# Optimization experiments

Measured on AMD Instinct MI355X. Metric: run time of the kernel, lower is better.

The kernel has to match this reference:

```python
import jax, jax.numpy as jnp
import numpy as np
import math

B, T, C = 2, 2048, 1024
N_HEADS = 16
HEAD_DIM = C // N_HEADS  # 64


def setup_inputs() -> dict:
    key = jax.random.key(0)
    ks = jax.random.split(key, 5)
    scale = 0.02
    return {
        "x": jax.random.normal(ks[0], (B, T, C), dtype=jnp.float32),
        "Wq": jax.random.normal(ks[1], (C, C), dtype=jnp.float32) * scale,
        "Wk": jax.random.normal(ks[2], (C, C), dtype=jnp.float32) * scale,
        "Wv": jax.random.normal(ks[3], (C, C), dtype=jnp.float32) * scale,
        "Wc": jax.random.normal(ks[4], (C, C), dtype=jnp.float32) * scale,
        "bc": jnp.zeros((C,), dtype=jnp.float32),
    }


def reference(x, Wq, Wk, Wv, Wc, bc):
    b, t, c = x.shape
    h, dh = N_HEADS, HEAD_DIM
    # Q/K/V projections (Linear, no bias): y = x @ W.T
    def proj(W):
        y = jnp.einsum('btc,dc->btd', x, W)
        return y.reshape(b, t, h, dh).transpose(0, 2, 1, 3)  # [B,H,T,dh]
    Q, K, V = proj(Wq), proj(Wk), proj(Wv)

    # scaled dot-product scores [B,H,T,T]
    scores = jnp.einsum('bhqd,bhkd->bhqk', Q, K) / math.sqrt(dh)
    # additive causal mask: + (1 - tril) * -1e9, as in the original
    causal = jnp.tril(jnp.ones((t, t), dtype=scores.dtype))
    scores = scores + (1.0 - causal) * (-1e9)

    attn = jax.nn.softmax(scores, axis=-1)  # dropout = identity (eval mode)
    o = jnp.einsum('bhqk,bhkd->bhqd', attn, V)
    o = o.transpose(0, 2, 1, 3).reshape(b, t, c)
    # output projection with bias (resid dropout = identity in eval)
    return jnp.einsum('btc,dc->btd', o, Wc) + bc
```

## Files before the change

kernel.cpp:

```cpp
#include <hip/hip_runtime.h>
#include <hip/hip_bf16.h>


typedef __attribute__((ext_vector_type(4))) float f32x4;
typedef __attribute__((ext_vector_type(4))) unsigned int u32x4;
typedef __attribute__((ext_vector_type(8))) __bf16 bf16x8;
typedef __attribute__((ext_vector_type(8))) unsigned short us8;
typedef __attribute__((ext_vector_type(4))) unsigned short us4;

#define LOG2E 1.4426950408889634f

__device__ __forceinline__ unsigned short f2bf(float f) {
    unsigned u = __builtin_bit_cast(unsigned, f);
    u += 0x7fffu + ((u >> 16) & 1u);
    return (unsigned short)(u >> 16);
}

__device__ __forceinline__ unsigned cvt_pk_bf16(float lo, float hi) {
    unsigned r;
    asm("v_cvt_pk_bf16_f32 %0, %1, %2" : "=v"(r) : "v"(lo), "v"(hi));
    return r;
}

__device__ __forceinline__ f32x4 mfma16(us8 a, us8 b, f32x4 c) {
    return __builtin_amdgcn_mfma_f32_16x16x32_bf16(
        __builtin_bit_cast(bf16x8, a), __builtin_bit_cast(bf16x8, b), c, 0, 0, 0);
}

__global__ __launch_bounds__(256) void fill_sentinel(float* __restrict__ out, int n) {
    int i = blockIdx.x * 256 + threadIdx.x;
    if (i < n) out[i] = 12345.0f;
}

__global__ __launch_bounds__(256) void cvt_x(const float* __restrict__ x,
                                             unsigned short* __restrict__ xb) {
    int idx = (blockIdx.x * 256 + threadIdx.x) * 4;
    f32x4 v = *(const f32x4*)(x + idx);
    us4 o = { f2bf(v[0]), f2bf(v[1]), f2bf(v[2]), f2bf(v[3]) };
    *(us4*)(xb + idx) = o;
}

template <bool AF32, bool BF32>
__device__ __forceinline__ void gemm_core(
    const void* __restrict__ Av, const void* __restrict__ Bv,
    int K, int m0, int n0, unsigned short* As, unsigned short* Bs, f32x4 acc[4][4]) {
    const float* Af = (const float*)Av;
    const unsigned short* Ab = (const unsigned short*)Av;
    const float* Bf = (const float*)Bv;
    const unsigned short* Bb = (const unsigned short*)Bv;
    const int tid = threadIdx.x;
    const int lane = tid & 63, wid = tid >> 6;
    const int g = lane >> 4, s = lane & 15;
    const int wr = wid >> 1, wc = wid & 1;
#pragma unroll
    for (int mi = 0; mi < 4; mi++)
#pragma unroll
        for (int ni = 0; ni < 4; ni++) acc[mi][ni] = (f32x4){0.f, 0.f, 0.f, 0.f};
    const int row = tid >> 3, col = (tid & 7) * 8;
    for (int k0 = 0; k0 < K; k0 += 64) {
        us8 av[4], bv[4];
#pragma unroll
        for (int p = 0; p < 4; p++) {
            size_t aoff = (size_t)(m0 + row + p * 32) * K + k0 + col;
            if (AF32) {
                f32x4 v0 = *(const f32x4*)(Af + aoff);
                f32x4 v1 = *(const f32x4*)(Af + aoff + 4);
                av[p] = (us8){ f2bf(v0[0]), f2bf(v0[1]), f2bf(v0[2]), f2bf(v0[3]),
                               f2bf(v1[0]), f2bf(v1[1]), f2bf(v1[2]), f2bf(v1[3]) };
            } else {
                av[p] = *(const us8*)(Ab + aoff);
            }
            size_t boff = (size_t)(n0 + row + p * 32) * K + k0 + col;
            if (BF32) {
                f32x4 v0 = *(const f32x4*)(Bf + boff);
                f32x4 v1 = *(const f32x4*)(Bf + boff + 4);
                bv[p] = (us8){ f2bf(v0[0]), f2bf(v0[1]), f2bf(v0[2]), f2bf(v0[3]),
                               f2bf(v1[0]), f2bf(v1[1]), f2bf(v1[2]), f2bf(v1[3]) };
            } else {
                bv[p] = *(const us8*)(Bb + boff);
            }
        }
        __syncthreads();
#pragma unroll
        for (int p = 0; p < 4; p++) {
            *(us8*)(As + (row + p * 32) * 72 + col) = av[p];
            *(us8*)(Bs + (row + p * 32) * 72 + col) = bv[p];
        }
        __syncthreads();
#pragma unroll
        for (int kk = 0; kk < 2; kk++) {
            us8 af[4], bf[4];
#pragma unroll
            for (int mi = 0; mi < 4; mi++)
                af[mi] = *(const us8*)(As + (wr * 64 + mi * 16 + s) * 72 + kk * 32 + g * 8);
#pragma unroll
            for (int ni = 0; ni < 4; ni++)
                bf[ni] = *(const us8*)(Bs + (wc * 64 + ni * 16 + s) * 72 + kk * 32 + g * 8);
#pragma unroll
            for (int mi = 0; mi < 4; mi++)
#pragma unroll
                for (int ni = 0; ni < 4; ni++)
                    acc[mi][ni] = mfma16(af[mi], bf[ni], acc[mi][ni]);
        }
    }
}

__global__ __launch_bounds__(256) void gemm_qkv(
    const unsigned short* __restrict__ X, const float* __restrict__ Wq,
    const float* __restrict__ Wk, const float* __restrict__ Wv,
    unsigned short* __restrict__ Qb, unsigned short* __restrict__ Kb,
    unsigned short* __restrict__ Vb) {
    __shared__ unsigned short As[128 * 72];
    __shared__ unsigned short Bs[128 * 72];
    const int bm = blockIdx.x & 31, bn = blockIdx.x >> 5;
    const int m0 = bm * 128;
    const int which = bn >> 3;
    const int n0 = (bn & 7) * 128;
    const float* W = which == 0 ? Wq : (which == 1 ? Wk : Wv);
    unsigned short* dst = which == 0 ? Qb : (which == 1 ? Kb : Vb);
    const float scale = which == 0 ? 0.125f : 1.0f;
    f32x4 acc[4][4];
    gemm_core<false, true>(X, W, 1024, m0, n0, As, Bs, acc);
    const int lane = threadIdx.x & 63, wid = threadIdx.x >> 6;
    const int g = lane >> 4, s = lane & 15, wr = wid >> 1, wc = wid & 1;
#pragma unroll
    for (int mi = 0; mi < 4; mi++)
#pragma unroll
        for (int ni = 0; ni < 4; ni++) {
            int n1 = n0 + wc * 64 + ni * 16 + s;
            int hh = n1 >> 6, dd = n1 & 63;
#pragma unroll
            for (int r = 0; r < 4; r++) {
                int mg = m0 + wr * 64 + mi * 16 + 4 * g + r;
                int bb = mg >> 11, tt = mg & 2047;
                dst[((size_t)(bb * 16 + hh) * 2048 + tt) * 64 + dd] = f2bf(acc[mi][ni][r] * scale);
            }
        }
}

__global__ __launch_bounds__(256) void transpose_v(
    const unsigned short* __restrict__ Vb, unsigned short* __restrict__ VtG) {
    __shared__ unsigned short T[64 * 68];
    const int bh = blockIdx.x >> 5, tt = blockIdx.x & 31;
    const int t0 = tt * 64;
    const unsigned short* src = Vb + (size_t)bh * 2048 * 64;
    unsigned short* dst = VtG + (size_t)bh * 64 * 2048;
    const int r = threadIdx.x >> 3, c = (threadIdx.x & 7) * 8;
#pragma unroll
    for (int p = 0; p < 2; p++) {
        us8 v = *(const us8*)(src + (size_t)(t0 + r + 32 * p) * 64 + c);
        *(us8*)(&T[(r + 32 * p) * 68 + c]) = v;
    }
    __syncthreads();
#pragma unroll
    for (int p = 0; p < 2; p++) {
        int d = r + 32 * p;
        us8 o;
#pragma unroll
        for (int j = 0; j < 8; j++) o[j] = T[(c + j) * 68 + d];
        *(us8*)(dst + (size_t)d * 2048 + t0 + c) = o;
    }
}

#define ATTN_EPILOGUE(QB0, OA, LR)                                              \
    {                                                                           \
        float li[4];                                                            \
        _Pragma("unroll") for (int r = 0; r < 4; r++)                           \
            li[r] = __shfl((LR), 4 * g + r, 64);                                \
        _Pragma("unroll") for (int db = 0; db < 4; db++)                        \
            _Pragma("unroll") for (int r = 0; r < 4; r++) {                     \
                int qq = (QB0) + 4 * g + r;                                     \
                float v = (OA)[db][r] / li[r];                                  \
                Ob[((size_t)(b * 2048) + qq) * 1024 + h * 64 + db * 16 + s] = f2bf(v); \
            }                                                                   \
    }

__global__ __launch_bounds__(256) void attn(
    const unsigned short* __restrict__ Qb, const unsigned short* __restrict__ Kb,
    const unsigned short* __restrict__ VtG, unsigned short* __restrict__ Ob) {
    __shared__ unsigned short Ks[64 * 72];
    __shared__ unsigned short Vt[64 * 72];
    const int bh = blockIdx.x >> 4, i = blockIdx.x & 15;
    const int b = bh >> 4, h = bh & 15;
    const unsigned short* Qp = Qb + (size_t)bh * 2048 * 64;
    const unsigned short* Kp = Kb + (size_t)bh * 2048 * 64;
    const unsigned short* Vp = VtG + (size_t)bh * 64 * 2048;
    const int tid = threadIdx.x, lane = tid & 63, wid = tid >> 6;
    const int g = lane >> 4, s = lane & 15;
    const int qbA = i * 64 + wid * 16;
    const int qbB = (31 - i) * 64 + wid * 16;
    const int qgA = qbA + s, qgB = qbB + s;
    us8 qfA[2], qfB[2];
    qfA[0] = *(const us8*)(Qp + (size_t)qgA * 64 + g * 8);
    qfA[1] = *(const us8*)(Qp + (size_t)qgA * 64 + 32 + g * 8);
    qfB[0] = *(const us8*)(Qp + (size_t)qgB * 64 + g * 8);
    qfB[1] = *(const us8*)(Qp + (size_t)qgB * 64 + 32 + g * 8);
    float m_run = -3.0e38f, l_run = 0.f;
    f32x4 o_acc[4];
#pragma unroll
    for (int db = 0; db < 4; db++) o_acc[db] = (f32x4){0.f, 0.f, 0.f, 0.f};
    const int srow = tid >> 3, scol = (tid & 7) * 8;
    us8 kpre[2], vpre[2];
#pragma unroll
    for (int p = 0; p < 2; p++) {
        kpre[p] = *(const us8*)(Kp + (size_t)(srow + 32 * p) * 64 + scol);
        vpre[p] = *(const us8*)(Vp + (size_t)(srow + 32 * p) * 2048 + scol);
    }
    for (int it = 0; it <= 32; ++it) {
        const bool qsel = it > i;
        const int kv0 = (qsel ? it - i - 1 : it) * 64;
        __syncthreads();
#pragma unroll
        for (int p = 0; p < 2; p++) {
            *(us8*)(Ks + (srow + 32 * p) * 72 + scol) = kpre[p];
            *(us8*)(Vt + (srow + 32 * p) * 72 + scol) = vpre[p];
        }
        __syncthreads();
        if (it < 32) {
            const int nx = it + 1;
            const int nkv0 = (nx > i ? nx - i - 1 : nx) * 64;
#pragma unroll
            for (int p = 0; p < 2; p++) {
                kpre[p] = *(const us8*)(Kp + (size_t)(nkv0 + srow + 32 * p) * 64 + scol);
                vpre[p] = *(const us8*)(Vp + (size_t)(srow + 32 * p) * 2048 + nkv0 + scol);
            }
        }
        if (it == i + 1) {
            ATTN_EPILOGUE(qbA, o_acc, l_run);
            m_run = -3.0e38f; l_run = 0.f;
#pragma unroll
            for (int db = 0; db < 4; db++) o_acc[db] = (f32x4){0.f, 0.f, 0.f, 0.f};
        }
        const int qg = qsel ? qgB : qgA;
        const us8* qf = qsel ? qfB : qfA;
        float sf[4][4];
        __builtin_amdgcn_s_setprio(1);
#pragma unroll
        for (int f = 0; f < 4; f++) {
            f32x4 a = (f32x4){0.f, 0.f, 0.f, 0.f};
            us8 k0v = *(const us8*)(Ks + (f * 16 + s) * 72 + g * 8);
            us8 k1v = *(const us8*)(Ks + (f * 16 + s) * 72 + 32 + g * 8);
            a = mfma16(k0v, qf[0], a);
            a = mfma16(k1v, qf[1], a);
#pragma unroll
            for (int r = 0; r < 4; r++) sf[f][r] = a[r];
        }
        __builtin_amdgcn_s_setprio(0);
        const bool diag = qsel ? (it == 32) : (it == i);
        if (diag) {
#pragma unroll
            for (int f = 0; f < 4; f++)
#pragma unroll
                for (int r = 0; r < 4; r++)
                    if (kv0 + f * 16 + 4 * g + r > qg) sf[f][r] = -3.0e38f;
        }
        float mt = -3.0e38f;
#pragma unroll
        for (int f = 0; f < 4; f++)
#pragma unroll
            for (int r = 0; r < 4; r++) mt = fmaxf(mt, sf[f][r]);
        mt = fmaxf(mt, __shfl_xor(mt, 16));
        mt = fmaxf(mt, __shfl_xor(mt, 32));
        float mnew = fmaxf(m_run, mt);
        float alpha = __builtin_amdgcn_exp2f((m_run - mnew) * LOG2E);
        float psum = 0.f;
#pragma unroll
        for (int f = 0; f < 4; f++)
#pragma unroll
            for (int r = 0; r < 4; r++) {
                float p = __builtin_amdgcn_exp2f((sf[f][r] - mnew) * LOG2E);
                sf[f][r] = p;
                psum += p;
            }
        psum += __shfl_xor(psum, 16);
        psum += __shfl_xor(psum, 32);
        l_run = l_run * alpha + psum;
        m_run = mnew;
        float al[4];
#pragma unroll
        for (int r = 0; r < 4; r++) al[r] = __shfl(alpha, 4 * g + r, 64);
#pragma unroll
        for (int db = 0; db < 4; db++)
#pragma unroll
            for (int r = 0; r < 4; r++) o_acc[db][r] *= al[r];
        unsigned pk[4][2];
#pragma unroll
        for (int f = 0; f < 4; f++)
#pragma unroll
            for (int hh2 = 0; hh2 < 2; hh2++)
                pk[f][hh2] = cvt_pk_bf16(sf[f][2 * hh2], sf[f][2 * hh2 + 1]);
        const int srcA = 32 * (g & 1) + s, srcB = srcA + 16;
        const bool ghi = g >= 2;
        us8 pa[2];
#pragma unroll
        for (int kk = 0; kk < 2; kk++) {
            unsigned e0 = __shfl(pk[kk * 2][0], srcA, 64);
            unsigned e1 = __shfl(pk[kk * 2][1], srcA, 64);
            unsigned e2 = __shfl(pk[kk * 2][0], srcB, 64);
            unsigned e3 = __shfl(pk[kk * 2][1], srcB, 64);
            unsigned o0 = __shfl(pk[kk * 2 + 1][0], srcA, 64);
            unsigned o1 = __shfl(pk[kk * 2 + 1][1], srcA, 64);
            unsigned o2 = __shfl(pk[kk * 2 + 1][0], srcB, 64);
            unsigned o3 = __shfl(pk[kk * 2 + 1][1], srcB, 64);
            u32x4 dw = { ghi ? o0 : e0, ghi ? o1 : e1, ghi ? o2 : e2, ghi ? o3 : e3 };
            pa[kk] = __builtin_bit_cast(us8, dw);
        }
        __builtin_amdgcn_s_setprio(1);
#pragma unroll
        for (int db = 0; db < 4; db++) {
            const unsigned short* vrow = Vt + (db * 16 + s) * 72;
            us8 vf0 = *(const us8*)(vrow + g * 8);
            o_acc[db] = mfma16(pa[0], vf0, o_acc[db]);
            us8 vf1 = *(const us8*)(vrow + 32 + g * 8);
            o_acc[db] = mfma16(pa[1], vf1, o_acc[db]);
        }
        __builtin_amdgcn_s_setprio(0);
    }
    ATTN_EPILOGUE(qbB, o_acc, l_run);
}

__global__ __launch_bounds__(256) void gemm_out(
    const unsigned short* __restrict__ O, const float* __restrict__ Wc,
    const float* __restrict__ bc, float* __restrict__ out) {
    __shared__ unsigned short As[128 * 72];
    __shared__ unsigned short Bs[128 * 72];
    const int bm = blockIdx.x & 31, bn = blockIdx.x >> 5;
    const int m0 = bm * 128, n0 = bn * 128;
    f32x4 acc[4][4];
    gemm_core<false, true>(O, Wc, 1024, m0, n0, As, Bs, acc);
    const int lane = threadIdx.x & 63, wid = threadIdx.x >> 6;
    const int g = lane >> 4, s = lane & 15, wr = wid >> 1, wc = wid & 1;
#pragma unroll
    for (int mi = 0; mi < 4; mi++)
#pragma unroll
        for (int ni = 0; ni < 4; ni++) {
            int ng = n0 + wc * 64 + ni * 16 + s;
            float bias = bc[ng];
#pragma unroll
            for (int r = 0; r < 4; r++) {
                int mg = m0 + wr * 64 + mi * 16 + 4 * g + r;
                out[(size_t)mg * 1024 + ng] = acc[mi][ni][r] + bias;
            }
        }
}

extern "C" void kernel_launch(void* const* d_in, const int* in_sizes, int n_in,
                              void* d_out, int out_size, void* d_ws, size_t ws_size,
                              hipStream_t stream) {
    const float* x  = (const float*)d_in[0];
    const float* Wq = (const float*)d_in[1];
    const float* Wk = (const float*)d_in[2];
    const float* Wv = (const float*)d_in[3];
    const float* Wc = (const float*)d_in[4];
    const float* bc = (const float*)d_in[5];
    float* out = (float*)d_out;

    if (ws_size < 33554432) {
        fill_sentinel<<<(out_size + 255) / 256, 256, 0, stream>>>(out, out_size);
        return;
    }
    char* w = (char*)d_ws;
    unsigned short* Qb = (unsigned short*)(w);
    unsigned short* Kb = (unsigned short*)(w + 8388608);
    unsigned short* Vb = (unsigned short*)(w + 16777216);
    unsigned short* Ob = (unsigned short*)(w + 25165824);
    unsigned short* VtG = (unsigned short*)d_out;
    unsigned short* xb  = (unsigned short*)((char*)d_out + 8388608);

    cvt_x<<<4096, 256, 0, stream>>>(x, xb);
    gemm_qkv<<<768, 256, 0, stream>>>(xb, Wq, Wk, Wv, Qb, Kb, Vb);
    transpose_v<<<1024, 256, 0, stream>>>(Vb, VtG);
    attn<<<512, 256, 0, stream>>>(Qb, Kb, VtG, Ob);
    gemm_out<<<256, 256, 0, stream>>>(Ob, Wc, bc, out);
}
```

Baseline: 134.6 us.

## Pre-convert weights to bf16, use direct global-to-LDS loads, lazy softmax rescale

```diff
diff --git a/kernel.cpp b/kernel.cpp
--- a/kernel.cpp
+++ b/kernel.cpp
@@ -27,27 +27,43 @@
         __builtin_bit_cast(bf16x8, a), __builtin_bit_cast(bf16x8, b), c, 0, 0, 0);
 }
 
+__device__ __forceinline__ void gload16(const unsigned short* gp, unsigned short* lp) {
+    __builtin_amdgcn_global_load_lds(
+        (const __attribute__((address_space(1))) void*)gp,
+        (__attribute__((address_space(3))) void*)lp, 16, 0, 0);
+}
+
 __global__ __launch_bounds__(256) void fill_sentinel(float* __restrict__ out, int n) {
     int i = blockIdx.x * 256 + threadIdx.x;
     if (i < n) out[i] = 12345.0f;
 }
 
-__global__ __launch_bounds__(256) void cvt_x(const float* __restrict__ x,
-                                             unsigned short* __restrict__ xb) {
+__global__ __launch_bounds__(256) void cvt_xw(
+    const float* __restrict__ x, const float* __restrict__ wq,
+    const float* __restrict__ wk, const float* __restrict__ wv,
+    unsigned short* __restrict__ xb, unsigned short* __restrict__ wqkvb) {
+    long i = (long)(blockIdx.x * 256 + threadIdx.x) * 4;
+    const float* src; unsigned short* dst; long off;
+    if (i < 4194304L)      { src = x;  dst = xb;              off = i; }
+    else if (i < 5242880L) { src = wq; dst = wqkvb;           off = i - 4194304L; }
+    else if (i < 6291456L) { src = wk; dst = wqkvb + 1048576; off = i - 5242880L; }
+    else                   { src = wv; dst = wqkvb + 2097152; off = i - 6291456L; }
+    f32x4 v = *(const f32x4*)(src + off);
+    us4 o = { f2bf(v[0]), f2bf(v[1]), f2bf(v[2]), f2bf(v[3]) };
+    *(us4*)(dst + off) = o;
+}
+
+__global__ __launch_bounds__(256) void cvt_wc(const float* __restrict__ wc,
+                                              unsigned short* __restrict__ wcb) {
     int idx = (blockIdx.x * 256 + threadIdx.x) * 4;
-    f32x4 v = *(const f32x4*)(x + idx);
+    f32x4 v = *(const f32x4*)(wc + idx);
     us4 o = { f2bf(v[0]), f2bf(v[1]), f2bf(v[2]), f2bf(v[3]) };
-    *(us4*)(xb + idx) = o;
-}
-
-template <bool AF32, bool BF32>
-__device__ __forceinline__ void gemm_core(
-    const void* __restrict__ Av, const void* __restrict__ Bv,
+    *(us4*)(wcb + idx) = o;
+}
+
+__device__ __forceinline__ void gemm_core_g(
+    const unsigned short* __restrict__ A, const unsigned short* __restrict__ B,
     int K, int m0, int n0, unsigned short* As, unsigned short* Bs, f32x4 acc[4][4]) {
-    const float* Af = (const float*)Av;
-    const unsigned short* Ab = (const unsigned short*)Av;
-    const float* Bf = (const float*)Bv;
-    const unsigned short* Bb = (const unsigned short*)Bv;
     const int tid = threadIdx.x;
     const int lane = tid & 63, wid = tid >> 6;
     const int g = lane >> 4, s = lane & 15;
@@ -56,35 +72,14 @@
     for (int mi = 0; mi < 4; mi++)
 #pragma unroll
         for (int ni = 0; ni < 4; ni++) acc[mi][ni] = (f32x4){0.f, 0.f, 0.f, 0.f};
-    const int row = tid >> 3, col = (tid & 7) * 8;
+    const int lrow = lane >> 3, lcol = (lane & 7) * 8;
     for (int k0 = 0; k0 < K; k0 += 64) {
-        us8 av[4], bv[4];
+        __syncthreads();
 #pragma unroll
         for (int p = 0; p < 4; p++) {
-            size_t aoff = (size_t)(m0 + row + p * 32) * K + k0 + col;
-            if (AF32) {
-                f32x4 v0 = *(const f32x4*)(Af + aoff);
-                f32x4 v1 = *(const f32x4*)(Af + aoff + 4);
-                av[p] = (us8){ f2bf(v0[0]), f2bf(v0[1]), f2bf(v0[2]), f2bf(v0[3]),
-                               f2bf(v1[0]), f2bf(v1[1]), f2bf(v1[2]), f2bf(v1[3]) };
-            } else {
-                av[p] = *(const us8*)(Ab + aoff);
-            }
-            size_t boff = (size_t)(n0 + row + p * 32) * K + k0 + col;
-            if (BF32) {
-                f32x4 v0 = *(const f32x4*)(Bf + boff);
-                f32x4 v1 = *(const f32x4*)(Bf + boff + 4);
-                bv[p] = (us8){ f2bf(v0[0]), f2bf(v0[1]), f2bf(v0[2]), f2bf(v0[3]),
-                               f2bf(v1[0]), f2bf(v1[1]), f2bf(v1[2]), f2bf(v1[3]) };
-            } else {
-                bv[p] = *(const us8*)(Bb + boff);
-            }
-        }
-        __syncthreads();
-#pragma unroll
-        for (int p = 0; p < 4; p++) {
-            *(us8*)(As + (row + p * 32) * 72 + col) = av[p];
-            *(us8*)(Bs + (row + p * 32) * 72 + col) = bv[p];
+            const int chunk = p * 4 + wid;
+            gload16(A + (size_t)(m0 + chunk * 8 + lrow) * K + k0 + lcol, As + chunk * 512);
+            gload16(B + (size_t)(n0 + chunk * 8 + lrow) * K + k0 + lcol, Bs + chunk * 512);
         }
         __syncthreads();
 #pragma unroll
@@ -92,10 +87,10 @@
             us8 af[4], bf[4];
 #pragma unroll
             for (int mi = 0; mi < 4; mi++)
-                af[mi] = *(const us8*)(As + (wr * 64 + mi * 16 + s) * 72 + kk * 32 + g * 8);
+                af[mi] = *(const us8*)(As + (wr * 64 + mi * 16 + s) * 64 + kk * 32 + g * 8);
 #pragma unroll
             for (int ni = 0; ni < 4; ni++)
-                bf[ni] = *(const us8*)(Bs + (wc * 64 + ni * 16 + s) * 72 + kk * 32 + g * 8);
+                bf[ni] = *(const us8*)(Bs + (wc * 64 + ni * 16 + s) * 64 + kk * 32 + g * 8);
 #pragma unroll
             for (int mi = 0; mi < 4; mi++)
 #pragma unroll
@@ -106,28 +101,25 @@
 }
 
 __global__ __launch_bounds__(256) void gemm_qkv(
-    const unsigned short* __restrict__ X, const float* __restrict__ Wq,
-    const float* __restrict__ Wk, const float* __restrict__ Wv,
+    const unsigned short* __restrict__ X, const unsigned short* __restrict__ W,
     unsigned short* __restrict__ Qb, unsigned short* __restrict__ Kb,
     unsigned short* __restrict__ Vb) {
-    __shared__ unsigned short As[128 * 72];
-    __shared__ unsigned short Bs[128 * 72];
+    __shared__ unsigned short As[128 * 64];
+    __shared__ unsigned short Bs[128 * 64];
     const int bm = blockIdx.x & 31, bn = blockIdx.x >> 5;
-    const int m0 = bm * 128;
-    const int which = bn >> 3;
-    const int n0 = (bn & 7) * 128;
-    const float* W = which == 0 ? Wq : (which == 1 ? Wk : Wv);
-    unsigned short* dst = which == 0 ? Qb : (which == 1 ? Kb : Vb);
-    const float scale = which == 0 ? 0.125f : 1.0f;
+    const int m0 = bm * 128, n0 = bn * 128;
     f32x4 acc[4][4];
-    gemm_core<false, true>(X, W, 1024, m0, n0, As, Bs, acc);
+    gemm_core_g(X, W, 1024, m0, n0, As, Bs, acc);
     const int lane = threadIdx.x & 63, wid = threadIdx.x >> 6;
     const int g = lane >> 4, s = lane & 15, wr = wid >> 1, wc = wid & 1;
 #pragma unroll
     for (int mi = 0; mi < 4; mi++)
 #pragma unroll
         for (int ni = 0; ni < 4; ni++) {
-            int n1 = n0 + wc * 64 + ni * 16 + s;
+            int ng = n0 + wc * 64 + ni * 16 + s;
+            int which = ng >> 10, n1 = ng & 1023;
+            unsigned short* dst = which == 0 ? Qb : (which == 1 ? Kb : Vb);
+            float scale = which == 0 ? 0.125f : 1.0f;
             int hh = n1 >> 6, dd = n1 & 63;
 #pragma unroll
             for (int r = 0; r < 4; r++) {
@@ -180,7 +172,7 @@
     const unsigned short* __restrict__ VtG, unsigned short* __restrict__ Ob) {
     __shared__ unsigned short Ks[64 * 72];
     __shared__ unsigned short Vt[64 * 72];
-    const int bh = blockIdx.x >> 4, i = blockIdx.x & 15;
+    const int bh = blockIdx.x & 31, i = blockIdx.x >> 5;
     const int b = bh >> 4, h = bh & 15;
     const unsigned short* Qp = Qb + (size_t)bh * 2048 * 64;
     const unsigned short* Kp = Kb + (size_t)bh * 2048 * 64;
@@ -261,8 +253,19 @@
             for (int r = 0; r < 4; r++) mt = fmaxf(mt, sf[f][r]);
         mt = fmaxf(mt, __shfl_xor(mt, 16));
         mt = fmaxf(mt, __shfl_xor(mt, 32));
-        float mnew = fmaxf(m_run, mt);
-        float alpha = __builtin_amdgcn_exp2f((m_run - mnew) * LOG2E);
+        float mnew = m_run;
+        if (!__all(mt - m_run <= 8.0f)) {
+            mnew = fmaxf(m_run, mt);
+            float alpha = __builtin_amdgcn_exp2f((m_run - mnew) * LOG2E);
+            l_run *= alpha;
+            float al[4];
+#pragma unroll
+            for (int r = 0; r < 4; r++) al[r] = __shfl(alpha, 4 * g + r, 64);
+#pragma unroll
+            for (int db = 0; db < 4; db++)
+#pragma unroll
+                for (int r = 0; r < 4; r++) o_acc[db][r] *= al[r];
+        }
         float psum = 0.f;
 #pragma unroll
         for (int f = 0; f < 4; f++)
@@ -274,15 +277,8 @@
             }
         psum += __shfl_xor(psum, 16);
         psum += __shfl_xor(psum, 32);
-        l_run = l_run * alpha + psum;
+        l_run += psum;
         m_run = mnew;
-        float al[4];
-#pragma unroll
-        for (int r = 0; r < 4; r++) al[r] = __shfl(alpha, 4 * g + r, 64);
-#pragma unroll
-        for (int db = 0; db < 4; db++)
-#pragma unroll
-            for (int r = 0; r < 4; r++) o_acc[db][r] *= al[r];
         unsigned pk[4][2];
 #pragma unroll
         for (int f = 0; f < 4; f++)
@@ -320,14 +316,14 @@
 }
 
 __global__ __launch_bounds__(256) void gemm_out(
-    const unsigned short* __restrict__ O, const float* __restrict__ Wc,
+    const unsigned short* __restrict__ O, const unsigned short* __restrict__ Wcb,
     const float* __restrict__ bc, float* __restrict__ out) {
-    __shared__ unsigned short As[128 * 72];
-    __shared__ unsigned short Bs[128 * 72];
+    __shared__ unsigned short As[128 * 64];
+    __shared__ unsigned short Bs[128 * 64];
     const int bm = blockIdx.x & 31, bn = blockIdx.x >> 5;
     const int m0 = bm * 128, n0 = bn * 128;
     f32x4 acc[4][4];
-    gemm_core<false, true>(O, Wc, 1024, m0, n0, As, Bs, acc);
+    gemm_core_g(O, Wcb, 1024, m0, n0, As, Bs, acc);
     const int lane = threadIdx.x & 63, wid = threadIdx.x >> 6;
     const int g = lane >> 4, s = lane & 15, wr = wid >> 1, wc = wid & 1;
 #pragma unroll
@@ -360,16 +356,19 @@
         return;
     }
     char* w = (char*)d_ws;
-    unsigned short* Qb = (unsigned short*)(w);
-    unsigned short* Kb = (unsigned short*)(w + 8388608);
-    unsigned short* Vb = (unsigned short*)(w + 16777216);
-    unsigned short* Ob = (unsigned short*)(w + 25165824);
-    unsigned short* VtG = (unsigned short*)d_out;
-    unsigned short* xb  = (unsigned short*)((char*)d_out + 8388608);
-
-    cvt_x<<<4096, 256, 0, stream>>>(x, xb);
-    gemm_qkv<<<768, 256, 0, stream>>>(xb, Wq, Wk, Wv, Qb, Kb, Vb);
+    unsigned short* Qb  = (unsigned short*)(w);
+    unsigned short* Kb  = (unsigned short*)(w + 8388608);
+    unsigned short* Vb  = (unsigned short*)(w + 16777216);
+    unsigned short* Ob  = (unsigned short*)(w + 25165824);
+    unsigned short* Wcb = (unsigned short*)(w + 16777216);
+    unsigned short* wqkvb = (unsigned short*)d_out;
+    unsigned short* VtG   = (unsigned short*)d_out;
+    unsigned short* xb    = (unsigned short*)((char*)d_out + 8388608);
+
+    cvt_xw<<<7168, 256, 0, stream>>>(x, Wq, Wk, Wv, xb, wqkvb);
+    gemm_qkv<<<768, 256, 0, stream>>>(xb, wqkvb, Qb, Kb, Vb);
     transpose_v<<<1024, 256, 0, stream>>>(Vb, VtG);
+    cvt_wc<<<1024, 256, 0, stream>>>(Wc, Wcb);
     attn<<<512, 256, 0, stream>>>(Qb, Kb, VtG, Ob);
-    gemm_out<<<256, 256, 0, stream>>>(Ob, Wc, bc, out);
-}
+    gemm_out<<<256, 256, 0, stream>>>(Ob, Wcb, bc, out);
+}
```

Result: slower. 142.0 us (+5.5%).

## Fuse V transpose into QKV GEMM, async A loads, rebalance attention and output GEMM

Applied to the files above, without the earlier changes.

```diff
diff --git a/kernel.cpp b/kernel.cpp
--- a/kernel.cpp
+++ b/kernel.cpp
@@ -25,6 +25,12 @@
 __device__ __forceinline__ f32x4 mfma16(us8 a, us8 b, f32x4 c) {
     return __builtin_amdgcn_mfma_f32_16x16x32_bf16(
         __builtin_bit_cast(bf16x8, a), __builtin_bit_cast(bf16x8, b), c, 0, 0, 0);
+}
+
+__device__ __forceinline__ void gload16(const unsigned short* gp, unsigned short* lp) {
+    __builtin_amdgcn_global_load_lds(
+        (const __attribute__((address_space(1))) void*)gp,
+        (__attribute__((address_space(3))) void*)lp, 16, 0, 0);
 }
 
 __global__ __launch_bounds__(256) void fill_sentinel(float* __restrict__ out, int n) {
@@ -40,64 +46,51 @@
     *(us4*)(xb + idx) = o;
 }
 
-template <bool AF32, bool BF32>
-__device__ __forceinline__ void gemm_core(
-    const void* __restrict__ Av, const void* __restrict__ Bv,
-    int K, int m0, int n0, unsigned short* As, unsigned short* Bs, f32x4 acc[4][4]) {
-    const float* Af = (const float*)Av;
-    const unsigned short* Ab = (const unsigned short*)Av;
-    const float* Bf = (const float*)Bv;
-    const unsigned short* Bb = (const unsigned short*)Bv;
+template <int MI>
+__device__ __forceinline__ void gemm_core_m(
+    const unsigned short* __restrict__ A, const float* __restrict__ Bf,
+    int K, int m0, int n0, unsigned short* As, unsigned short* Bs, f32x4 acc[MI][4]) {
     const int tid = threadIdx.x;
     const int lane = tid & 63, wid = tid >> 6;
     const int g = lane >> 4, s = lane & 15;
     const int wr = wid >> 1, wc = wid & 1;
 #pragma unroll
-    for (int mi = 0; mi < 4; mi++)
+    for (int mi = 0; mi < MI; mi++)
 #pragma unroll
         for (int ni = 0; ni < 4; ni++) acc[mi][ni] = (f32x4){0.f, 0.f, 0.f, 0.f};
-    const int row = tid >> 3, col = (tid & 7) * 8;
+    const int lrow = lane >> 3, lcol = (lane & 7) * 8;
+    const int brow = tid >> 3, bcol = (tid & 7) * 8;
     for (int k0 = 0; k0 < K; k0 += 64) {
-        us8 av[4], bv[4];
+        us8 bv[4];
 #pragma unroll
         for (int p = 0; p < 4; p++) {
-            size_t aoff = (size_t)(m0 + row + p * 32) * K + k0 + col;
-            if (AF32) {
-                f32x4 v0 = *(const f32x4*)(Af + aoff);
-                f32x4 v1 = *(const f32x4*)(Af + aoff + 4);
-                av[p] = (us8){ f2bf(v0[0]), f2bf(v0[1]), f2bf(v0[2]), f2bf(v0[3]),
-                               f2bf(v1[0]), f2bf(v1[1]), f2bf(v1[2]), f2bf(v1[3]) };
-            } else {
-                av[p] = *(const us8*)(Ab + aoff);
-            }
-            size_t boff = (size_t)(n0 + row + p * 32) * K + k0 + col;
-            if (BF32) {
-                f32x4 v0 = *(const f32x4*)(Bf + boff);
-                f32x4 v1 = *(const f32x4*)(Bf + boff + 4);
-                bv[p] = (us8){ f2bf(v0[0]), f2bf(v0[1]), f2bf(v0[2]), f2bf(v0[3]),
-                               f2bf(v1[0]), f2bf(v1[1]), f2bf(v1[2]), f2bf(v1[3]) };
-            } else {
-                bv[p] = *(const us8*)(Bb + boff);
-            }
+            size_t boff = (size_t)(n0 + brow + p * 32) * K + k0 + bcol;
+            f32x4 v0 = *(const f32x4*)(Bf + boff);
+            f32x4 v1 = *(const f32x4*)(Bf + boff + 4);
+            bv[p] = (us8){ f2bf(v0[0]), f2bf(v0[1]), f2bf(v0[2]), f2bf(v0[3]),
+                           f2bf(v1[0]), f2bf(v1[1]), f2bf(v1[2]), f2bf(v1[3]) };
         }
         __syncthreads();
 #pragma unroll
-        for (int p = 0; p < 4; p++) {
-            *(us8*)(As + (row + p * 32) * 72 + col) = av[p];
-            *(us8*)(Bs + (row + p * 32) * 72 + col) = bv[p];
-        }
+        for (int p = 0; p < MI; p++) {
+            const int chunk = p * 4 + wid;
+            gload16(A + (size_t)(m0 + chunk * 8 + lrow) * K + k0 + lcol, As + chunk * 512);
+        }
+#pragma unroll
+        for (int p = 0; p < 4; p++)
+            *(us8*)(Bs + (brow + p * 32) * 72 + bcol) = bv[p];
         __syncthreads();
 #pragma unroll
         for (int kk = 0; kk < 2; kk++) {
-            us8 af[4], bf[4];
-#pragma unroll
-            for (int mi = 0; mi < 4; mi++)
-                af[mi] = *(const us8*)(As + (wr * 64 + mi * 16 + s) * 72 + kk * 32 + g * 8);
+            us8 af[MI], bf[4];
+#pragma unroll
+            for (int mi = 0; mi < MI; mi++)
+                af[mi] = *(const us8*)(As + (wr * (MI * 16) + mi * 16 + s) * 64 + kk * 32 + g * 8);
 #pragma unroll
             for (int ni = 0; ni < 4; ni++)
                 bf[ni] = *(const us8*)(Bs + (wc * 64 + ni * 16 + s) * 72 + kk * 32 + g * 8);
 #pragma unroll
-            for (int mi = 0; mi < 4; mi++)
+            for (int mi = 0; mi < MI; mi++)
 #pragma unroll
                 for (int ni = 0; ni < 4; ni++)
                     acc[mi][ni] = mfma16(af[mi], bf[ni], acc[mi][ni]);
@@ -109,20 +102,19 @@
     const unsigned short* __restrict__ X, const float* __restrict__ Wq,
     const float* __restrict__ Wk, const float* __restrict__ Wv,
     unsigned short* __restrict__ Qb, unsigned short* __restrict__ Kb,
-    unsigned short* __restrict__ Vb) {
-    __shared__ unsigned short As[128 * 72];
+    unsigned short* __restrict__ VtG) {
+    __shared__ unsigned short As[128 * 64];
     __shared__ unsigned short Bs[128 * 72];
     const int bm = blockIdx.x & 31, bn = blockIdx.x >> 5;
     const int m0 = bm * 128;
     const int which = bn >> 3;
     const int n0 = (bn & 7) * 128;
     const float* W = which == 0 ? Wq : (which == 1 ? Wk : Wv);
-    unsigned short* dst = which == 0 ? Qb : (which == 1 ? Kb : Vb);
-    const float scale = which == 0 ? 0.125f : 1.0f;
     f32x4 acc[4][4];
-    gemm_core<false, true>(X, W, 1024, m0, n0, As, Bs, acc);
+    gemm_core_m<4>(X, W, 1024, m0, n0, As, Bs, acc);
     const int lane = threadIdx.x & 63, wid = threadIdx.x >> 6;
     const int g = lane >> 4, s = lane & 15, wr = wid >> 1, wc = wid & 1;
+    const float scale = which == 0 ? 0.125f : 1.0f;
 #pragma unroll
     for (int mi = 0; mi < 4; mi++)
 #pragma unroll
@@ -133,68 +125,36 @@
             for (int r = 0; r < 4; r++) {
                 int mg = m0 + wr * 64 + mi * 16 + 4 * g + r;
                 int bb = mg >> 11, tt = mg & 2047;
-                dst[((size_t)(bb * 16 + hh) * 2048 + tt) * 64 + dd] = f2bf(acc[mi][ni][r] * scale);
+                unsigned short v = f2bf(acc[mi][ni][r] * scale);
+                if (which == 0)
+                    Qb[((size_t)(bb * 16 + hh) * 2048 + tt) * 64 + dd] = v;
+                else if (which == 1)
+                    Kb[((size_t)(bb * 16 + hh) * 2048 + tt) * 64 + dd] = v;
+                else
+                    VtG[((size_t)(bb * 16 + hh) * 64 + dd) * 2048 + tt] = v;
             }
         }
 }
-
-__global__ __launch_bounds__(256) void transpose_v(
-    const unsigned short* __restrict__ Vb, unsigned short* __restrict__ VtG) {
-    __shared__ unsigned short T[64 * 68];
-    const int bh = blockIdx.x >> 5, tt = blockIdx.x & 31;
-    const int t0 = tt * 64;
-    const unsigned short* src = Vb + (size_t)bh * 2048 * 64;
-    unsigned short* dst = VtG + (size_t)bh * 64 * 2048;
-    const int r = threadIdx.x >> 3, c = (threadIdx.x & 7) * 8;
-#pragma unroll
-    for (int p = 0; p < 2; p++) {
-        us8 v = *(const us8*)(src + (size_t)(t0 + r + 32 * p) * 64 + c);
-        *(us8*)(&T[(r + 32 * p) * 68 + c]) = v;
-    }
-    __syncthreads();
-#pragma unroll
-    for (int p = 0; p < 2; p++) {
-        int d = r + 32 * p;
-        us8 o;
-#pragma unroll
-        for (int j = 0; j < 8; j++) o[j] = T[(c + j) * 68 + d];
-        *(us8*)(dst + (size_t)d * 2048 + t0 + c) = o;
-    }
-}
-
-#define ATTN_EPILOGUE(QB0, OA, LR)                                              \
-    {                                                                           \
-        float li[4];                                                            \
-        _Pragma("unroll") for (int r = 0; r < 4; r++)                           \
-            li[r] = __shfl((LR), 4 * g + r, 64);                                \
-        _Pragma("unroll") for (int db = 0; db < 4; db++)                        \
-            _Pragma("unroll") for (int r = 0; r < 4; r++) {                     \
-                int qq = (QB0) + 4 * g + r;                                     \
-                float v = (OA)[db][r] / li[r];                                  \
-                Ob[((size_t)(b * 2048) + qq) * 1024 + h * 64 + db * 16 + s] = f2bf(v); \
-            }                                                                   \
-    }
 
 __global__ __launch_bounds__(256) void attn(
     const unsigned short* __restrict__ Qb, const unsigned short* __restrict__ Kb,
     const unsigned short* __restrict__ VtG, unsigned short* __restrict__ Ob) {
     __shared__ unsigned short Ks[64 * 72];
     __shared__ unsigned short Vt[64 * 72];
-    const int bh = blockIdx.x >> 4, i = blockIdx.x & 15;
+    const int bh = blockIdx.x & 31, j = blockIdx.x >> 5;
+    const int q4 = j & 7, sel = j >> 3;
+    const int i = sel == 0 ? q4 : (sel == 1 ? 15 - q4 : (sel == 2 ? 16 + q4 : 31 - q4));
     const int b = bh >> 4, h = bh & 15;
     const unsigned short* Qp = Qb + (size_t)bh * 2048 * 64;
     const unsigned short* Kp = Kb + (size_t)bh * 2048 * 64;
     const unsigned short* Vp = VtG + (size_t)bh * 64 * 2048;
     const int tid = threadIdx.x, lane = tid & 63, wid = tid >> 6;
     const int g = lane >> 4, s = lane & 15;
-    const int qbA = i * 64 + wid * 16;
-    const int qbB = (31 - i) * 64 + wid * 16;
-    const int qgA = qbA + s, qgB = qbB + s;
-    us8 qfA[2], qfB[2];
-    qfA[0] = *(const us8*)(Qp + (size_t)qgA * 64 + g * 8);
-    qfA[1] = *(const us8*)(Qp + (size_t)qgA * 64 + 32 + g * 8);
-    qfB[0] = *(const us8*)(Qp + (size_t)qgB * 64 + g * 8);
-    qfB[1] = *(const us8*)(Qp + (size_t)qgB * 64 + 32 + g * 8);
+    const int qb0 = i * 64 + wid * 16;
+    const int qg = qb0 + s;
+    us8 qf[2];
+    qf[0] = *(const us8*)(Qp + (size_t)qg * 64 + g * 8);
+    qf[1] = *(const us8*)(Qp + (size_t)qg * 64 + 32 + g * 8);
     float m_run = -3.0e38f, l_run = 0.f;
     f32x4 o_acc[4];
 #pragma unroll
@@ -206,9 +166,8 @@
         kpre[p] = *(const us8*)(Kp + (size_t)(srow + 32 * p) * 64 + scol);
         vpre[p] = *(const us8*)(Vp + (size_t)(srow + 32 * p) * 2048 + scol);
     }
-    for (int it = 0; it <= 32; ++it) {
-        const bool qsel = it > i;
-        const int kv0 = (qsel ? it - i - 1 : it) * 64;
+    for (int it = 0; it <= i; ++it) {
+        const int kv0 = it * 64;
         __syncthreads();
 #pragma unroll
         for (int p = 0; p < 2; p++) {
@@ -216,23 +175,14 @@
             *(us8*)(Vt + (srow + 32 * p) * 72 + scol) = vpre[p];
         }
         __syncthreads();
-        if (it < 32) {
-            const int nx = it + 1;
-            const int nkv0 = (nx > i ? nx - i - 1 : nx) * 64;
+        if (it < i) {
+            const int nkv0 = kv0 + 64;
 #pragma unroll
             for (int p = 0; p < 2; p++) {
                 kpre[p] = *(const us8*)(Kp + (size_t)(nkv0 + srow + 32 * p) * 64 + scol);
                 vpre[p] = *(const us8*)(Vp + (size_t)(srow + 32 * p) * 2048 + nkv0 + scol);
             }
         }
-        if (it == i + 1) {
-            ATTN_EPILOGUE(qbA, o_acc, l_run);
-            m_run = -3.0e38f; l_run = 0.f;
-#pragma unroll
-            for (int db = 0; db < 4; db++) o_acc[db] = (f32x4){0.f, 0.f, 0.f, 0.f};
-        }
-        const int qg = qsel ? qgB : qgA;
-        const us8* qf = qsel ? qfB : qfA;
         float sf[4][4];
         __builtin_amdgcn_s_setprio(1);
 #pragma unroll
@@ -246,8 +196,7 @@
             for (int r = 0; r < 4; r++) sf[f][r] = a[r];
         }
         __builtin_amdgcn_s_setprio(0);
-        const bool diag = qsel ? (it == 32) : (it == i);
-        if (diag) {
+        if (it == i) {
 #pragma unroll
             for (int f = 0; f < 4; f++)
 #pragma unroll
@@ -261,8 +210,19 @@
             for (int r = 0; r < 4; r++) mt = fmaxf(mt, sf[f][r]);
         mt = fmaxf(mt, __shfl_xor(mt, 16));
         mt = fmaxf(mt, __shfl_xor(mt, 32));
-        float mnew = fmaxf(m_run, mt);
-        float alpha = __builtin_amdgcn_exp2f((m_run - mnew) * LOG2E);
+        float mnew = m_run;
+        if (!__all(mt - m_run <= 8.0f)) {
+            mnew = fmaxf(m_run, mt);
+            float alpha = __builtin_amdgcn_exp2f((m_run - mnew) * LOG2E);
+            l_run *= alpha;
+            float al[4];
+#pragma unroll
+            for (int r = 0; r < 4; r++) al[r] = __shfl(alpha, 4 * g + r, 64);
+#pragma unroll
+            for (int db = 0; db < 4; db++)
+#pragma unroll
+                for (int r = 0; r < 4; r++) o_acc[db][r] *= al[r];
+        }
         float psum = 0.f;
 #pragma unroll
         for (int f = 0; f < 4; f++)
@@ -274,15 +234,8 @@
             }
         psum += __shfl_xor(psum, 16);
         psum += __shfl_xor(psum, 32);
-        l_run = l_run * alpha + psum;
+        l_run += psum;
         m_run = mnew;
-        float al[4];
-#pragma unroll
-        for (int r = 0; r < 4; r++) al[r] = __shfl(alpha, 4 * g + r, 64);
-#pragma unroll
-        for (int db = 0; db < 4; db++)
-#pragma unroll
-            for (int r = 0; r < 4; r++) o_acc[db][r] *= al[r];
         unsigned pk[4][2];
 #pragma unroll
         for (int f = 0; f < 4; f++)
@@ -316,29 +269,39 @@
         }
         __builtin_amdgcn_s_setprio(0);
     }
-    ATTN_EPILOGUE(qbB, o_acc, l_run);
+    float li[4];
+#pragma unroll
+    for (int r = 0; r < 4; r++) li[r] = __shfl(l_run, 4 * g + r, 64);
+#pragma unroll
+    for (int db = 0; db < 4; db++)
+#pragma unroll
+        for (int r = 0; r < 4; r++) {
+            int qq = qb0 + 4 * g + r;
+            float v = o_acc[db][r] / li[r];
+            Ob[((size_t)(b * 2048) + qq) * 1024 + h * 64 + db * 16 + s] = f2bf(v);
+        }
 }
 
 __global__ __launch_bounds__(256) void gemm_out(
     const unsigned short* __restrict__ O, const float* __restrict__ Wc,
     const float* __restrict__ bc, float* __restrict__ out) {
-    __shared__ unsigned short As[128 * 72];
+    __shared__ unsigned short As[64 * 64];
     __shared__ unsigned short Bs[128 * 72];
-    const int bm = blockIdx.x & 31, bn = blockIdx.x >> 5;
-    const int m0 = bm * 128, n0 = bn * 128;
-    f32x4 acc[4][4];
-    gemm_core<false, true>(O, Wc, 1024, m0, n0, As, Bs, acc);
+    const int bm = blockIdx.x & 63, bn = blockIdx.x >> 6;
+    const int m0 = bm * 64, n0 = bn * 128;
+    f32x4 acc[2][4];
+    gemm_core_m<2>(O, Wc, 1024, m0, n0, As, Bs, acc);
     const int lane = threadIdx.x & 63, wid = threadIdx.x >> 6;
     const int g = lane >> 4, s = lane & 15, wr = wid >> 1, wc = wid & 1;
 #pragma unroll
-    for (int mi = 0; mi < 4; mi++)
+    for (int mi = 0; mi < 2; mi++)
 #pragma unroll
         for (int ni = 0; ni < 4; ni++) {
             int ng = n0 + wc * 64 + ni * 16 + s;
             float bias = bc[ng];
 #pragma unroll
             for (int r = 0; r < 4; r++) {
-                int mg = m0 + wr * 64 + mi * 16 + 4 * g + r;
+                int mg = m0 + wr * 32 + mi * 16 + 4 * g + r;
                 out[(size_t)mg * 1024 + ng] = acc[mi][ni][r] + bias;
             }
         }
@@ -360,16 +323,14 @@
         return;
     }
     char* w = (char*)d_ws;
-    unsigned short* Qb = (unsigned short*)(w);
-    unsigned short* Kb = (unsigned short*)(w + 8388608);
-    unsigned short* Vb = (unsigned short*)(w + 16777216);
-    unsigned short* Ob = (unsigned short*)(w + 25165824);
-    unsigned short* VtG = (unsigned short*)d_out;
-    unsigned short* xb  = (unsigned short*)((char*)d_out + 8388608);
+    unsigned short* Qb  = (unsigned short*)(w);
+    unsigned short* Kb  = (unsigned short*)(w + 8388608);
+    unsigned short* VtG = (unsigned short*)(w + 16777216);
+    unsigned short* Ob  = (unsigned short*)(w + 25165824);
+    unsigned short* xb  = (unsigned short*)d_out;
 
     cvt_x<<<4096, 256, 0, stream>>>(x, xb);
-    gemm_qkv<<<768, 256, 0, stream>>>(xb, Wq, Wk, Wv, Qb, Kb, Vb);
-    transpose_v<<<1024, 256, 0, stream>>>(Vb, VtG);
-    attn<<<512, 256, 0, stream>>>(Qb, Kb, VtG, Ob);
-    gemm_out<<<256, 256, 0, stream>>>(Ob, Wc, bc, out);
-}
+    gemm_qkv<<<768, 256, 0, stream>>>(xb, Wq, Wk, Wv, Qb, Kb, VtG);
+    attn<<<1024, 256, 0, stream>>>(Qb, Kb, VtG, Ob);
+    gemm_out<<<512, 256, 0, stream>>>(Ob, Wc, bc, out);
+}
```

Result: slower. 141.5 us (+5.1%).
